# Kernel tuning notes

Measured on AMD Instinct MI355X. Metric: run time of the kernel, lower is better.

The kernel has to match this reference:

```python
import jax, jax.numpy as jnp
import numpy as np

DIM = 512
HEADS = 8


def setup_inputs() -> dict:
    key = jax.random.key(0)
    k1, k2, k3, k4 = jax.random.split(key, 4)
    head_dim = DIM // HEADS
    scale = head_dim ** -0.5
    x = jax.random.normal(k1, (4, 4096, DIM), dtype=jnp.float32)
    Wqkv = jax.random.normal(k2, (3 * DIM, DIM), dtype=jnp.float32) * (DIM ** -0.5)
    temperature = jnp.ones((HEADS, 1, 1), dtype=jnp.float32) * scale
    Wproj = jax.random.normal(k3, (DIM, DIM), dtype=jnp.float32) * (DIM ** -0.5)
    bproj = jnp.zeros((DIM,), dtype=jnp.float32)
    return {"x": x, "Wqkv": Wqkv, "temperature": temperature, "Wproj": Wproj, "bproj": bproj}


def reference(x, Wqkv, temperature, Wproj, bproj):
    B, N, C = x.shape
    H = temperature.shape[0]
    D = C // H
    qkv = (x @ Wqkv.T).reshape(B, N, 3, H, D).transpose(2, 0, 3, 1, 4)  # (3,B,H,N,D)
    q, k, v = qkv[0], qkv[1], qkv[2]
    q = jax.nn.relu(q)
    k = jax.nn.relu(k)
    # denom = clamp(q @ sum_n k, min=100) -> (B,H,N,1)
    ksum = k.sum(axis=2)  # (B,H,D)
    denom = jnp.clip(jnp.einsum('bhnd,bhd->bhn', q, ksum), 100.0)[..., None]
    # attn = (k^T v) * temperature -> (B,H,D,D)
    attn = jnp.einsum('bhnd,bhne->bhde', k, v) * temperature
    attn1 = jnp.einsum('bhnd,bhde->bhne', q, attn)  # (B,H,N,D)
    out = attn1 / denom
    y = out.transpose(0, 2, 1, 3).reshape(B, N, C) @ Wproj.T + bproj
    return (y, attn1)
```

## Files before the change

kernel.cpp:

```cpp
#include <hip/hip_runtime.h>
#include <cstdint>
#include <cstddef>

typedef _Float16 f16;
typedef _Float16 f16x4 __attribute__((ext_vector_type(4)));
typedef _Float16 f16x8 __attribute__((ext_vector_type(8)));
typedef float f32x4 __attribute__((ext_vector_type(4)));

#define MFMA16(a, b, c) __builtin_amdgcn_mfma_f32_16x16x32_f16(a, b, c, 0, 0, 0)

static __device__ __forceinline__ void gld16(const void* g, void* l) {
  __builtin_amdgcn_global_load_lds(
      (const __attribute__((address_space(1))) void*)g,
      (__attribute__((address_space(3))) void*)l, 16, 0, 0);
}

#define B_ 4
#define N_ 4096
#define C_ 512
#define H_ 8
#define D_ 64
#define BN_ROWS 16384
#define QKV_COLS 1536

__global__ __launch_bounds__(256) void k_convert(
    const float* __restrict__ x, const float* __restrict__ wqkv,
    const float* __restrict__ wproj,
    f16* __restrict__ xh, f16* __restrict__ wqkvh, f16* __restrict__ wprojh)
{
  const int NX  = (BN_ROWS * C_) / 4;
  const int NW1 = (QKV_COLS * C_) / 4;
  const int NW2 = (C_ * C_) / 4;
  const int total = NX + NW1 + NW2;
  const int stride = gridDim.x * blockDim.x;
  for (int i = blockIdx.x * blockDim.x + threadIdx.x; i < total; i += stride) {
    const float4* s; f16x4* d; int j;
    if (i < NX)              { s = (const float4*)x;     d = (f16x4*)xh;     j = i; }
    else if (i < NX + NW1)   { s = (const float4*)wqkv;  d = (f16x4*)wqkvh;  j = i - NX; }
    else                     { s = (const float4*)wproj; d = (f16x4*)wprojh; j = i - NX - NW1; }
    float4 v = s[j];
    f16x4 o; o[0] = (f16)v.x; o[1] = (f16)v.y; o[2] = (f16)v.z; o[3] = (f16)v.w;
    d[j] = o;
  }
}

__global__ __launch_bounds__(256) void k_qkv_gemm(
    const f16* __restrict__ X, const f16* __restrict__ W, f16* __restrict__ Out)
{
  __shared__ f16 As[128][64];
  __shared__ f16 Bs[128][64];
  int w = (blockIdx.x & 7) * 192 + (blockIdx.x >> 3);
  const int n0 = (w % 12) * 128;
  const int m0 = (w / 12) * 128;
  const int tid = threadIdx.x;
  const int wid = tid >> 6;
  const int lane = tid & 63;
  const int lr = lane & 15, lg = lane >> 4;
  const int sr = lane >> 3;
  const int sslot = (lane & 7) ^ sr;
  const int wr = (wid >> 1) * 64, wc = (wid & 1) * 64;
  f32x4 acc[4][4] = {};
  for (int kt = 0; kt < 512; kt += 64) {
#pragma unroll
    for (int i = 0; i < 4; ++i) {
      int chunk = wid * 4 + i;
      int row = chunk * 8 + sr;
      gld16(&X[(size_t)(m0 + row) * 512 + kt + sslot * 8], &As[chunk * 8][0]);
      gld16(&W[(size_t)(n0 + row) * 512 + kt + sslot * 8], &Bs[chunk * 8][0]);
    }
    __syncthreads();
#pragma unroll
    for (int kk = 0; kk < 2; ++kk) {
      f16x8 af[4], bf[4];
#pragma unroll
      for (int m = 0; m < 4; ++m)
        af[m] = *(const f16x8*)&As[wr + m * 16 + lr][(((kk * 4 + lg) ^ (lr & 7)) * 8)];
#pragma unroll
      for (int n = 0; n < 4; ++n)
        bf[n] = *(const f16x8*)&Bs[wc + n * 16 + lr][(((kk * 4 + lg) ^ (lr & 7)) * 8)];
#pragma unroll
      for (int m = 0; m < 4; ++m)
#pragma unroll
        for (int n = 0; n < 4; ++n)
          acc[m][n] = MFMA16(bf[n], af[m], acc[m][n]);
    }
    __syncthreads();
  }
#pragma unroll
  for (int m = 0; m < 4; ++m)
#pragma unroll
    for (int n = 0; n < 4; ++n) {
      int row = m0 + wr + m * 16 + lr;
      int col = n0 + wc + n * 16 + lg * 4;
      f16x4 o;
      bool relu = (col < 1024);
#pragma unroll
      for (int j = 0; j < 4; ++j) {
        float v = acc[m][n][j];
        if (relu) v = fmaxf(v, 0.f);
        o[j] = (f16)v;
      }
      *(f16x4*)&Out[(size_t)row * QKV_COLS + col] = o;
    }
}

__global__ __launch_bounds__(256) void k_ktv(
    const f16* __restrict__ qkv, float* __restrict__ partial, float* __restrict__ pksum)
{
  __shared__ f16 ks[32][64];
  __shared__ f16 vs[32][64];
  const int bh = blockIdx.x, sp = blockIdx.y;
  const int b = bh >> 3, h = bh & 7;
  const int tid = threadIdx.x, wid = tid >> 6, lane = tid & 63;
  const int srow = lane >> 3, scol = (lane & 7) * 8;
  const int td = (wid << 2) | (lane >> 4);
  const int te = lane & 15;
  float acc[4][4] = {};
  float ksacc[4] = {0.f, 0.f, 0.f, 0.f};
  const size_t rowbase = (size_t)b * N_ + sp * 128;
  for (int t = 0; t < 4; ++t) {
    int nb = t * 32 + wid * 8 + srow;
    gld16(&qkv[(rowbase + nb) * QKV_COLS + 512 + h * 64 + scol], &ks[wid * 8][0]);
    gld16(&qkv[(rowbase + nb) * QKV_COLS + 1024 + h * 64 + scol], &vs[wid * 8][0]);
    __syncthreads();
#pragma unroll 4
    for (int n = 0; n < 32; ++n) {
      f16x4 kd = *(const f16x4*)&ks[n][td * 4];
      f16x4 ve = *(const f16x4*)&vs[n][te * 4];
      float kf[4], vf[4];
#pragma unroll
      for (int i = 0; i < 4; ++i) { kf[i] = (float)kd[i]; vf[i] = (float)ve[i]; }
#pragma unroll
      for (int i = 0; i < 4; ++i)
#pragma unroll
        for (int j = 0; j < 4; ++j)
          acc[i][j] += kf[i] * vf[j];
      if (te == 0) {
#pragma unroll
        for (int i = 0; i < 4; ++i) ksacc[i] += kf[i];
      }
    }
    __syncthreads();
  }
  float* pp = partial + (size_t)(bh * 32 + sp) * 4096;
#pragma unroll
  for (int i = 0; i < 4; ++i)
#pragma unroll
    for (int j = 0; j < 4; ++j)
      pp[(td * 4 + i) * 64 + te * 4 + j] = acc[i][j];
  if (te == 0) {
    float* kp = pksum + (bh * 32 + sp) * 64;
#pragma unroll
    for (int i = 0; i < 4; ++i) kp[td * 4 + i] = ksacc[i];
  }
}

__global__ __launch_bounds__(256) void k_reduce(
    const float* __restrict__ partial, const float* __restrict__ pksum,
    float* __restrict__ attn_acc, float* __restrict__ ksum)
{
  const int bh = blockIdx.x, seg = blockIdx.y, tid = threadIdx.x;
  const int i = seg * 256 + tid;
  float s = 0.f;
#pragma unroll 8
  for (int sp = 0; sp < 32; ++sp) s += partial[(size_t)(bh * 32 + sp) * 4096 + i];
  attn_acc[bh * 4096 + i] = s;
  if (seg == 0 && tid < 64) {
    float t2 = 0.f;
#pragma unroll 8
    for (int sp = 0; sp < 32; ++sp) t2 += pksum[(bh * 32 + sp) * 64 + tid];
    ksum[bh * 64 + tid] = t2;
  }
}

__global__ __launch_bounds__(256) void k_attn1(
    const f16* __restrict__ qkv, const float* __restrict__ attn_acc,
    const float* __restrict__ ksum, const float* __restrict__ temp,
    float* __restrict__ attn1_out, f16* __restrict__ outh)
{
  __shared__ f16 attnT[64][64];
  __shared__ float ksum_s[64];
  __shared__ float denom_s[256];
  const int bh = blockIdx.x, sp = blockIdx.y;
  const int b = bh >> 3, h = bh & 7;
  const int tid = threadIdx.x, wid = tid >> 6, lane = tid & 63;
  const int lr = lane & 15, lg = lane >> 4;
  const int n0 = sp * 256;
  const float tscale = temp[h];
  {
    int e = tid & 63, dblk = (tid >> 6) * 16;
    float vals[16];
#pragma unroll
    for (int x = 0; x < 16; ++x)
      vals[x] = attn_acc[bh * 4096 + (dblk + x) * 64 + e] * tscale;
#pragma unroll
    for (int half = 0; half < 2; ++half) {
      int slot = ((dblk >> 3) + half) ^ (e & 7);
      f16x8 pk;
#pragma unroll
      for (int j = 0; j < 8; ++j) pk[j] = (f16)vals[half * 8 + j];
      *(f16x8*)&attnT[e][slot * 8] = pk;
    }
  }
  if (tid < 64) ksum_s[tid] = ksum[bh * 64 + tid];
  __syncthreads();
  {
    size_t row = (size_t)b * N_ + n0 + tid;
    const f16* qrow = &qkv[row * QKV_COLS + h * 64];
    float dot = 0.f;
#pragma unroll
    for (int d0 = 0; d0 < 64; d0 += 8) {
      f16x8 qv = *(const f16x8*)&qrow[d0];
#pragma unroll
      for (int j = 0; j < 8; ++j) dot += (float)qv[j] * ksum_s[d0 + j];
    }
    denom_s[tid] = fmaxf(dot, 100.f);
  }
  f16x8 bf[4][2];
#pragma unroll
  for (int et = 0; et < 4; ++et)
#pragma unroll
    for (int kk = 0; kk < 2; ++kk) {
      int e = et * 16 + lr;
      bf[et][kk] = *(const f16x8*)&attnT[e][(((kk * 4 + lg) ^ (e & 7)) * 8)];
    }
  __syncthreads();
  f32x4 acc[4][4] = {};
#pragma unroll
  for (int mt = 0; mt < 4; ++mt) {
    size_t rbase = ((size_t)b * N_ + n0 + wid * 64 + mt * 16 + lr) * QKV_COLS + h * 64;
#pragma unroll
    for (int kk = 0; kk < 2; ++kk) {
      f16x8 a = *(const f16x8*)&qkv[rbase + kk * 32 + lg * 8];
#pragma unroll
      for (int et = 0; et < 4; ++et)
        acc[mt][et] = MFMA16(bf[et][kk], a, acc[mt][et]);
    }
  }
#pragma unroll
  for (int mt = 0; mt < 4; ++mt) {
    int rl = wid * 64 + mt * 16 + lr;
    int n = n0 + rl;
    float dn = denom_s[rl];
#pragma unroll
    for (int et = 0; et < 4; ++et) {
      int e = et * 16 + lg * 4;
      float4 o;
      f16x4 oh;
      o.x = acc[mt][et][0]; o.y = acc[mt][et][1]; o.z = acc[mt][et][2]; o.w = acc[mt][et][3];
#pragma unroll
      for (int j = 0; j < 4; ++j) oh[j] = (f16)(acc[mt][et][j] / dn);
      *(float4*)&attn1_out[((size_t)bh * N_ + n) * 64 + e] = o;
      *(f16x4*)&outh[((size_t)b * N_ + n) * 512 + h * 64 + e] = oh;
    }
  }
}

__global__ __launch_bounds__(256) void k_proj_gemm(
    const f16* __restrict__ X, const f16* __restrict__ W,
    const float* __restrict__ bias, float* __restrict__ Y)
{
  __shared__ f16 As[128][64];
  __shared__ f16 Bs[128][64];
  int w = (blockIdx.x & 7) * 64 + (blockIdx.x >> 3);
  const int n0 = (w % 4) * 128;
  const int m0 = (w / 4) * 128;
  const int tid = threadIdx.x;
  const int wid = tid >> 6;
  const int lane = tid & 63;
  const int lr = lane & 15, lg = lane >> 4;
  const int sr = lane >> 3;
  const int sslot = (lane & 7) ^ sr;
  const int wr = (wid >> 1) * 64, wc = (wid & 1) * 64;
  f32x4 acc[4][4] = {};
  for (int kt = 0; kt < 512; kt += 64) {
#pragma unroll
    for (int i = 0; i < 4; ++i) {
      int chunk = wid * 4 + i;
      int row = chunk * 8 + sr;
      gld16(&X[(size_t)(m0 + row) * 512 + kt + sslot * 8], &As[chunk * 8][0]);
      gld16(&W[(size_t)(n0 + row) * 512 + kt + sslot * 8], &Bs[chunk * 8][0]);
    }
    __syncthreads();
#pragma unroll
    for (int kk = 0; kk < 2; ++kk) {
      f16x8 af[4], bf[4];
#pragma unroll
      for (int m = 0; m < 4; ++m)
        af[m] = *(const f16x8*)&As[wr + m * 16 + lr][(((kk * 4 + lg) ^ (lr & 7)) * 8)];
#pragma unroll
      for (int n = 0; n < 4; ++n)
        bf[n] = *(const f16x8*)&Bs[wc + n * 16 + lr][(((kk * 4 + lg) ^ (lr & 7)) * 8)];
#pragma unroll
      for (int m = 0; m < 4; ++m)
#pragma unroll
        for (int n = 0; n < 4; ++n)
          acc[m][n] = MFMA16(bf[n], af[m], acc[m][n]);
    }
    __syncthreads();
  }
#pragma unroll
  for (int m = 0; m < 4; ++m)
#pragma unroll
    for (int n = 0; n < 4; ++n) {
      int row = m0 + wr + m * 16 + lr;
      int col = n0 + wc + n * 16 + lg * 4;
      float4 o;
      o.x = acc[m][n][0] + bias[col + 0];
      o.y = acc[m][n][1] + bias[col + 1];
      o.z = acc[m][n][2] + bias[col + 2];
      o.w = acc[m][n][3] + bias[col + 3];
      *(float4*)&Y[(size_t)row * C_ + col] = o;
    }
}

extern "C" void kernel_launch(void* const* d_in, const int* in_sizes, int n_in,
                              void* d_out, int out_size, void* d_ws, size_t ws_size,
                              hipStream_t stream)
{
  const float* x     = (const float*)d_in[0];
  const float* wqkv  = (const float*)d_in[1];
  const float* temp  = (const float*)d_in[2];
  const float* wproj = (const float*)d_in[3];
  const float* bproj = (const float*)d_in[4];
  float* y_out     = (float*)d_out;
  float* attn1_out = (float*)d_out + 8388608;

  char* ws = (char*)d_ws;
  f16*   xh       = (f16*)(ws);
  float* partial  = (float*)(ws);
  f16*   wqkvh    = (f16*)(ws + 16777216);
  f16*   wprojh   = (f16*)(ws + 18350080);
  f16*   qkvh     = (f16*)(ws + 18874368);
  float* attn_acc = (float*)(ws + 69206016);
  float* ksum     = (float*)(ws + 69730304);
  float* pksum    = (float*)(ws + 69738496);
  f16*   outh     = (f16*)(ws + 70000640);

  hipLaunchKernelGGL(k_convert,  dim3(2048),    dim3(256), 0, stream, x, wqkv, wproj, xh, wqkvh, wprojh);
  hipLaunchKernelGGL(k_qkv_gemm, dim3(1536),    dim3(256), 0, stream, xh, wqkvh, qkvh);
  hipLaunchKernelGGL(k_ktv,      dim3(32, 32),  dim3(256), 0, stream, qkvh, partial, pksum);
  hipLaunchKernelGGL(k_reduce,   dim3(32, 16),  dim3(256), 0, stream, partial, pksum, attn_acc, ksum);
  hipLaunchKernelGGL(k_attn1,    dim3(32, 16),  dim3(256), 0, stream, qkvh, attn_acc, ksum, temp, attn1_out, outh);
  hipLaunchKernelGGL(k_proj_gemm,dim3(512),     dim3(256), 0, stream, outh, wprojh, bproj, y_out);
}
```

Baseline: 123.1 us.

## Replace both GEMMs with 256x128-tile, 8-wave, 4-slot pipelined templated kernel

Both GEMM kernels are replaced by one templated kernel with 256x128 output tiles, 512 threads and a four-slot LDS ring. Loads are issued two k-steps ahead using direct global-to-LDS transfers, and waiting uses explicit vmcnt counters with a single barrier per step. MFMA sections get raised wave priority. The goal is to hide global load latency and halve the barrier count per k-tile. In exchange the XOR swizzle is dropped, so LDS reads may hit bank conflicts, and the proj GEMM now launches only 256 blocks, which may underfill the GPU.

```diff
diff --git a/kernel.cpp b/kernel.cpp
--- a/kernel.cpp
+++ b/kernel.cpp
@@ -44,64 +44,112 @@
   }
 }
 
-__global__ __launch_bounds__(256) void k_qkv_gemm(
-    const f16* __restrict__ X, const f16* __restrict__ W, f16* __restrict__ Out)
-{
-  __shared__ f16 As[128][64];
-  __shared__ f16 Bs[128][64];
-  int w = (blockIdx.x & 7) * 192 + (blockIdx.x >> 3);
-  const int n0 = (w % 12) * 128;
-  const int m0 = (w / 12) * 128;
+template<int NTN, int BPX, int MODE>
+__global__ __launch_bounds__(512, 2) void k_gemm8(
+    const f16* __restrict__ A, const f16* __restrict__ Bm,
+    const float* __restrict__ bias, f16* __restrict__ OutH,
+    float* __restrict__ OutF)
+{
+  constexpr int BM = 256, BN = 128;
+  constexpr int SLOT = (BM + BN) * 32;
+  __shared__ f16 lds[4 * SLOT];
+
+  int w = (blockIdx.x & 7) * BPX + (blockIdx.x >> 3);
+  const int m0 = (w / NTN) * BM;
+  const int n0 = (w % NTN) * BN;
   const int tid = threadIdx.x;
-  const int wid = tid >> 6;
-  const int lane = tid & 63;
+  const int wid = tid >> 6, lane = tid & 63;
   const int lr = lane & 15, lg = lane >> 4;
-  const int sr = lane >> 3;
-  const int sslot = (lane & 7) ^ sr;
-  const int wr = (wid >> 1) * 64, wc = (wid & 1) * 64;
+  const int wm = wid >> 1, wn = wid & 1;
+
+  const int strow = lane >> 2, stslot = (lane & 3) * 8;
+
   f32x4 acc[4][4] = {};
-  for (int kt = 0; kt < 512; kt += 64) {
-#pragma unroll
-    for (int i = 0; i < 4; ++i) {
-      int chunk = wid * 4 + i;
-      int row = chunk * 8 + sr;
-      gld16(&X[(size_t)(m0 + row) * 512 + kt + sslot * 8], &As[chunk * 8][0]);
-      gld16(&W[(size_t)(n0 + row) * 512 + kt + sslot * 8], &Bs[chunk * 8][0]);
-    }
-    __syncthreads();
-#pragma unroll
-    for (int kk = 0; kk < 2; ++kk) {
-      f16x8 af[4], bf[4];
-#pragma unroll
-      for (int m = 0; m < 4; ++m)
-        af[m] = *(const f16x8*)&As[wr + m * 16 + lr][(((kk * 4 + lg) ^ (lr & 7)) * 8)];
+
+#define STAGE(tt, s)                                                          \
+  do {                                                                        \
+    f16* lbase = lds + (s) * SLOT;                                            \
+    _Pragma("unroll")                                                         \
+    for (int r = 0; r < 2; ++r) {                                             \
+      int row = r * 128 + wid * 16;                                           \
+      gld16(&A[(size_t)(m0 + row + strow) * 512 + (tt) * 32 + stslot],        \
+            lbase + row * 32);                                                \
+    }                                                                         \
+    {                                                                         \
+      int row = wid * 16;                                                     \
+      gld16(&Bm[(size_t)(n0 + row + strow) * 512 + (tt) * 32 + stslot],       \
+            lbase + BM * 32 + row * 32);                                      \
+    }                                                                         \
+  } while (0)
+
+  STAGE(0, 0);
+  STAGE(1, 1);
+  asm volatile("s_waitcnt vmcnt(3)" ::: "memory");
+  __builtin_amdgcn_s_barrier();
+  asm volatile("" ::: "memory");
+
+#pragma unroll
+  for (int t = 0; t < 16; ++t) {
+    if (t + 2 < 16) STAGE(t + 2, (t + 2) & 3);
+    const f16* base = lds + (t & 3) * SLOT;
+    f16x8 af[4], bf[4];
+#pragma unroll
+    for (int m = 0; m < 4; ++m)
+      af[m] = *(const f16x8*)(base + (wm * 64 + m * 16 + lr) * 32 + lg * 8);
+#pragma unroll
+    for (int n = 0; n < 4; ++n)
+      bf[n] = *(const f16x8*)(base + BM * 32 + (wn * 64 + n * 16 + lr) * 32 + lg * 8);
+    __builtin_amdgcn_s_setprio(1);
+#pragma unroll
+    for (int m = 0; m < 4; ++m)
 #pragma unroll
       for (int n = 0; n < 4; ++n)
-        bf[n] = *(const f16x8*)&Bs[wc + n * 16 + lr][(((kk * 4 + lg) ^ (lr & 7)) * 8)];
-#pragma unroll
-      for (int m = 0; m < 4; ++m)
-#pragma unroll
-        for (int n = 0; n < 4; ++n)
-          acc[m][n] = MFMA16(bf[n], af[m], acc[m][n]);
-    }
-    __syncthreads();
-  }
-#pragma unroll
-  for (int m = 0; m < 4; ++m)
-#pragma unroll
-    for (int n = 0; n < 4; ++n) {
-      int row = m0 + wr + m * 16 + lr;
-      int col = n0 + wc + n * 16 + lg * 4;
-      f16x4 o;
-      bool relu = (col < 1024);
-#pragma unroll
-      for (int j = 0; j < 4; ++j) {
-        float v = acc[m][n][j];
-        if (relu) v = fmaxf(v, 0.f);
-        o[j] = (f16)v;
+        acc[m][n] = MFMA16(bf[n], af[m], acc[m][n]);
+    __builtin_amdgcn_s_setprio(0);
+    if (t < 14) {
+      asm volatile("s_waitcnt vmcnt(3)" ::: "memory");
+    } else if (t == 14) {
+      asm volatile("s_waitcnt vmcnt(0)" ::: "memory");
+    }
+    if (t < 15) {
+      __builtin_amdgcn_s_barrier();
+      asm volatile("" ::: "memory");
+    }
+  }
+#undef STAGE
+
+  if (MODE == 0) {
+    const bool relu = (n0 < 1024);
+#pragma unroll
+    for (int m = 0; m < 4; ++m)
+#pragma unroll
+      for (int n = 0; n < 4; ++n) {
+        int row = m0 + wm * 64 + m * 16 + lr;
+        int col = n0 + wn * 64 + n * 16 + lg * 4;
+        f16x4 o;
+#pragma unroll
+        for (int j = 0; j < 4; ++j) {
+          float v = acc[m][n][j];
+          if (relu) v = fmaxf(v, 0.f);
+          o[j] = (f16)v;
+        }
+        *(f16x4*)&OutH[(size_t)row * QKV_COLS + col] = o;
       }
-      *(f16x4*)&Out[(size_t)row * QKV_COLS + col] = o;
-    }
+  } else {
+#pragma unroll
+    for (int m = 0; m < 4; ++m)
+#pragma unroll
+      for (int n = 0; n < 4; ++n) {
+        int row = m0 + wm * 64 + m * 16 + lr;
+        int col = n0 + wn * 64 + n * 16 + lg * 4;
+        float4 o;
+        o.x = acc[m][n][0] + bias[col + 0];
+        o.y = acc[m][n][1] + bias[col + 1];
+        o.z = acc[m][n][2] + bias[col + 2];
+        o.w = acc[m][n][3] + bias[col + 3];
+        *(float4*)&OutF[(size_t)row * C_ + col] = o;
+      }
+  }
 }
 
 __global__ __launch_bounds__(256) void k_ktv(
@@ -256,64 +304,6 @@
   }
 }
 
-__global__ __launch_bounds__(256) void k_proj_gemm(
-    const f16* __restrict__ X, const f16* __restrict__ W,
-    const float* __restrict__ bias, float* __restrict__ Y)
-{
-  __shared__ f16 As[128][64];
-  __shared__ f16 Bs[128][64];
-  int w = (blockIdx.x & 7) * 64 + (blockIdx.x >> 3);
-  const int n0 = (w % 4) * 128;
-  const int m0 = (w / 4) * 128;
-  const int tid = threadIdx.x;
-  const int wid = tid >> 6;
-  const int lane = tid & 63;
-  const int lr = lane & 15, lg = lane >> 4;
-  const int sr = lane >> 3;
-  const int sslot = (lane & 7) ^ sr;
-  const int wr = (wid >> 1) * 64, wc = (wid & 1) * 64;
-  f32x4 acc[4][4] = {};
-  for (int kt = 0; kt < 512; kt += 64) {
-#pragma unroll
-    for (int i = 0; i < 4; ++i) {
-      int chunk = wid * 4 + i;
-      int row = chunk * 8 + sr;
-      gld16(&X[(size_t)(m0 + row) * 512 + kt + sslot * 8], &As[chunk * 8][0]);
-      gld16(&W[(size_t)(n0 + row) * 512 + kt + sslot * 8], &Bs[chunk * 8][0]);
-    }
-    __syncthreads();
-#pragma unroll
-    for (int kk = 0; kk < 2; ++kk) {
-      f16x8 af[4], bf[4];
-#pragma unroll
-      for (int m = 0; m < 4; ++m)
-        af[m] = *(const f16x8*)&As[wr + m * 16 + lr][(((kk * 4 + lg) ^ (lr & 7)) * 8)];
-#pragma unroll
-      for (int n = 0; n < 4; ++n)
-        bf[n] = *(const f16x8*)&Bs[wc + n * 16 + lr][(((kk * 4 + lg) ^ (lr & 7)) * 8)];
-#pragma unroll
-      for (int m = 0; m < 4; ++m)
-#pragma unroll
-        for (int n = 0; n < 4; ++n)
-          acc[m][n] = MFMA16(bf[n], af[m], acc[m][n]);
-    }
-    __syncthreads();
-  }
-#pragma unroll
-  for (int m = 0; m < 4; ++m)
-#pragma unroll
-    for (int n = 0; n < 4; ++n) {
-      int row = m0 + wr + m * 16 + lr;
-      int col = n0 + wc + n * 16 + lg * 4;
-      float4 o;
-      o.x = acc[m][n][0] + bias[col + 0];
-      o.y = acc[m][n][1] + bias[col + 1];
-      o.z = acc[m][n][2] + bias[col + 2];
-      o.w = acc[m][n][3] + bias[col + 3];
-      *(float4*)&Y[(size_t)row * C_ + col] = o;
-    }
-}
-
 extern "C" void kernel_launch(void* const* d_in, const int* in_sizes, int n_in,
                               void* d_out, int out_size, void* d_ws, size_t ws_size,
                               hipStream_t stream)
@@ -338,9 +328,11 @@
   f16*   outh     = (f16*)(ws + 70000640);
 
   hipLaunchKernelGGL(k_convert,  dim3(2048),    dim3(256), 0, stream, x, wqkv, wproj, xh, wqkvh, wprojh);
-  hipLaunchKernelGGL(k_qkv_gemm, dim3(1536),    dim3(256), 0, stream, xh, wqkvh, qkvh);
+  hipLaunchKernelGGL((k_gemm8<12, 96, 0>), dim3(768), dim3(512), 0, stream,
+                     xh, wqkvh, (const float*)nullptr, qkvh, (float*)nullptr);
   hipLaunchKernelGGL(k_ktv,      dim3(32, 32),  dim3(256), 0, stream, qkvh, partial, pksum);
   hipLaunchKernelGGL(k_reduce,   dim3(32, 16),  dim3(256), 0, stream, partial, pksum, attn_acc, ksum);
   hipLaunchKernelGGL(k_attn1,    dim3(32, 16),  dim3(256), 0, stream, qkvh, attn_acc, ksum, temp, attn1_out, outh);
-  hipLaunchKernelGGL(k_proj_gemm,dim3(512),     dim3(256), 0, stream, outh, wprojh, bproj, y_out);
-}
+  hipLaunchKernelGGL((k_gemm8<4, 32, 1>), dim3(256), dim3(512), 0, stream,
+                     outh, wprojh, bproj, (f16*)nullptr, y_out);
+}
```

Measured after the change: 128.4 us. 1.04x slower.

## Fuse fp32-to-fp16 x conversion into QKV GEMM and double-buffer both GEMMs

Applied to the files above, without the earlier changes.

The QKV GEMM now reads fp32 x directly into registers, converts it to fp16 and writes it to swizzled LDS. This removes the separate conversion pass over x, which wrote a 16 MB fp16 copy and then read it back. Both GEMMs gain double-buffered LDS with prefetch of the next K tile while MFMAs run on the current one. They also use manual waitcnt/barrier control and setprio around the MFMA block. The trade-off is more LDS per block (64 KB), register-staged A loads in the QKV GEMM, and fragile hand-written vmcnt accounting.

```diff
diff --git a/kernel.cpp b/kernel.cpp
--- a/kernel.cpp
+++ b/kernel.cpp
@@ -24,76 +24,127 @@
 #define QKV_COLS 1536
 
 __global__ __launch_bounds__(256) void k_convert(
-    const float* __restrict__ x, const float* __restrict__ wqkv,
-    const float* __restrict__ wproj,
-    f16* __restrict__ xh, f16* __restrict__ wqkvh, f16* __restrict__ wprojh)
-{
-  const int NX  = (BN_ROWS * C_) / 4;
+    const float* __restrict__ wqkv, const float* __restrict__ wproj,
+    f16* __restrict__ wqkvh, f16* __restrict__ wprojh)
+{
   const int NW1 = (QKV_COLS * C_) / 4;
   const int NW2 = (C_ * C_) / 4;
-  const int total = NX + NW1 + NW2;
+  const int total = NW1 + NW2;
   const int stride = gridDim.x * blockDim.x;
   for (int i = blockIdx.x * blockDim.x + threadIdx.x; i < total; i += stride) {
     const float4* s; f16x4* d; int j;
-    if (i < NX)              { s = (const float4*)x;     d = (f16x4*)xh;     j = i; }
-    else if (i < NX + NW1)   { s = (const float4*)wqkv;  d = (f16x4*)wqkvh;  j = i - NX; }
-    else                     { s = (const float4*)wproj; d = (f16x4*)wprojh; j = i - NX - NW1; }
+    if (i < NW1) { s = (const float4*)wqkv;  d = (f16x4*)wqkvh;  j = i; }
+    else         { s = (const float4*)wproj; d = (f16x4*)wprojh; j = i - NW1; }
     float4 v = s[j];
     f16x4 o; o[0] = (f16)v.x; o[1] = (f16)v.y; o[2] = (f16)v.z; o[3] = (f16)v.w;
     d[j] = o;
   }
 }
 
-__global__ __launch_bounds__(256) void k_qkv_gemm(
-    const f16* __restrict__ X, const f16* __restrict__ W, f16* __restrict__ Out)
-{
-  __shared__ f16 As[128][64];
-  __shared__ f16 Bs[128][64];
+__global__ __launch_bounds__(256, 2) void k_qkv_gemm(
+    const float* __restrict__ X, const f16* __restrict__ W, f16* __restrict__ Out)
+{
+  __shared__ f16 As[2][128][64];
+  __shared__ f16 Bs[2][128][64];
   int w = (blockIdx.x & 7) * 192 + (blockIdx.x >> 3);
+  const int m0 = (w / 12) * 128;
   const int n0 = (w % 12) * 128;
-  const int m0 = (w / 12) * 128;
   const int tid = threadIdx.x;
-  const int wid = tid >> 6;
-  const int lane = tid & 63;
+  const int wid = tid >> 6, lane = tid & 63;
   const int lr = lane & 15, lg = lane >> 4;
-  const int sr = lane >> 3;
-  const int sslot = (lane & 7) ^ sr;
-  const int wr = (wid >> 1) * 64, wc = (wid & 1) * 64;
+  const int wm = wid >> 1, wn = wid & 1;
+  const int sr = lane >> 3, sslot = (lane & 7) ^ sr;
+  const int arow = tid >> 1;
+  const float* asrc = &X[(size_t)(m0 + arow) * 512 + (tid & 1) * 32];
+  float4 areg[8];
   f32x4 acc[4][4] = {};
-  for (int kt = 0; kt < 512; kt += 64) {
-#pragma unroll
-    for (int i = 0; i < 4; ++i) {
-      int chunk = wid * 4 + i;
-      int row = chunk * 8 + sr;
-      gld16(&X[(size_t)(m0 + row) * 512 + kt + sslot * 8], &As[chunk * 8][0]);
-      gld16(&W[(size_t)(n0 + row) * 512 + kt + sslot * 8], &Bs[chunk * 8][0]);
-    }
-    __syncthreads();
+
+#define STAGE_B(tt, q)                                                        \
+  do {                                                                        \
+    _Pragma("unroll")                                                         \
+    for (int i = 0; i < 4; ++i) {                                             \
+      int chunk = wid * 4 + i;                                                \
+      gld16(&W[(size_t)(n0 + chunk * 8 + sr) * 512 + (tt) * 64 + sslot * 8],  \
+            &Bs[q][chunk * 8][0]);                                            \
+    }                                                                         \
+  } while (0)
+#define LOADA(tt)                                                             \
+  do {                                                                        \
+    _Pragma("unroll")                                                         \
+    for (int j = 0; j < 8; ++j)                                               \
+      areg[j] = *(const float4*)(asrc + (tt) * 64 + j * 4);                   \
+  } while (0)
+#define WRITEA(q)                                                             \
+  do {                                                                        \
+    _Pragma("unroll")                                                         \
+    for (int p2 = 0; p2 < 4; ++p2) {                                          \
+      int slot = (tid & 1) * 4 + p2;                                          \
+      f16x8 pk;                                                               \
+      pk[0] = (f16)areg[2*p2].x;   pk[1] = (f16)areg[2*p2].y;                 \
+      pk[2] = (f16)areg[2*p2].z;   pk[3] = (f16)areg[2*p2].w;                 \
+      pk[4] = (f16)areg[2*p2+1].x; pk[5] = (f16)areg[2*p2+1].y;               \
+      pk[6] = (f16)areg[2*p2+1].z; pk[7] = (f16)areg[2*p2+1].w;               \
+      *(f16x8*)&As[q][arow][((slot ^ (arow & 7)) * 8)] = pk;                  \
+    }                                                                         \
+  } while (0)
+
+  STAGE_B(0, 0);
+  LOADA(0);
+  asm volatile("s_waitcnt vmcnt(0)" ::: "memory");
+  WRITEA(0);
+  LOADA(1);
+  asm volatile("s_waitcnt lgkmcnt(0)" ::: "memory");
+  __builtin_amdgcn_s_barrier();
+  asm volatile("" ::: "memory");
+
+#pragma unroll
+  for (int t = 0; t < 8; ++t) {
+    const int p = t & 1, q = p ^ 1;
+    if (t < 7) STAGE_B(t + 1, q);
+    f16x8 af[2][4], bf[2][4];
 #pragma unroll
     for (int kk = 0; kk < 2; ++kk) {
-      f16x8 af[4], bf[4];
 #pragma unroll
       for (int m = 0; m < 4; ++m)
-        af[m] = *(const f16x8*)&As[wr + m * 16 + lr][(((kk * 4 + lg) ^ (lr & 7)) * 8)];
+        af[kk][m] = *(const f16x8*)&As[p][wm * 64 + m * 16 + lr][(((kk * 4 + lg) ^ (lr & 7)) * 8)];
 #pragma unroll
       for (int n = 0; n < 4; ++n)
-        bf[n] = *(const f16x8*)&Bs[wc + n * 16 + lr][(((kk * 4 + lg) ^ (lr & 7)) * 8)];
+        bf[kk][n] = *(const f16x8*)&Bs[p][wn * 64 + n * 16 + lr][(((kk * 4 + lg) ^ (lr & 7)) * 8)];
+    }
+    if (t < 7) {
+      asm volatile("s_waitcnt vmcnt(4)" ::: "memory");
+      WRITEA(q);
+      if (t < 6) LOADA(t + 2);
+    }
+    __builtin_amdgcn_s_setprio(1);
+#pragma unroll
+    for (int kk = 0; kk < 2; ++kk)
 #pragma unroll
       for (int m = 0; m < 4; ++m)
 #pragma unroll
         for (int n = 0; n < 4; ++n)
-          acc[m][n] = MFMA16(bf[n], af[m], acc[m][n]);
-    }
-    __syncthreads();
-  }
+          acc[m][n] = MFMA16(bf[kk][n], af[kk][m], acc[m][n]);
+    __builtin_amdgcn_s_setprio(0);
+    if (t < 7) {
+      asm volatile("s_waitcnt lgkmcnt(0)" ::: "memory");
+      if (t < 6) asm volatile("s_waitcnt vmcnt(8)" ::: "memory");
+      else       asm volatile("s_waitcnt vmcnt(0)" ::: "memory");
+      __builtin_amdgcn_s_barrier();
+      asm volatile("" ::: "memory");
+    }
+  }
+#undef STAGE_B
+#undef LOADA
+#undef WRITEA
+
+  const bool relu = (n0 < 1024);
 #pragma unroll
   for (int m = 0; m < 4; ++m)
 #pragma unroll
     for (int n = 0; n < 4; ++n) {
-      int row = m0 + wr + m * 16 + lr;
-      int col = n0 + wc + n * 16 + lg * 4;
+      int row = m0 + wm * 64 + m * 16 + lr;
+      int col = n0 + wn * 64 + n * 16 + lg * 4;
       f16x4 o;
-      bool relu = (col < 1024);
 #pragma unroll
       for (int j = 0; j < 4; ++j) {
         float v = acc[m][n][j];
@@ -256,55 +307,77 @@
   }
 }
 
-__global__ __launch_bounds__(256) void k_proj_gemm(
-    const f16* __restrict__ X, const f16* __restrict__ W,
+__global__ __launch_bounds__(256, 2) void k_proj_gemm(
+    const f16* __restrict__ Xh, const f16* __restrict__ W,
     const float* __restrict__ bias, float* __restrict__ Y)
 {
-  __shared__ f16 As[128][64];
-  __shared__ f16 Bs[128][64];
+  __shared__ f16 As[2][128][64];
+  __shared__ f16 Bs[2][128][64];
   int w = (blockIdx.x & 7) * 64 + (blockIdx.x >> 3);
+  const int m0 = (w / 4) * 128;
   const int n0 = (w % 4) * 128;
-  const int m0 = (w / 4) * 128;
   const int tid = threadIdx.x;
-  const int wid = tid >> 6;
-  const int lane = tid & 63;
+  const int wid = tid >> 6, lane = tid & 63;
   const int lr = lane & 15, lg = lane >> 4;
-  const int sr = lane >> 3;
-  const int sslot = (lane & 7) ^ sr;
-  const int wr = (wid >> 1) * 64, wc = (wid & 1) * 64;
+  const int wm = wid >> 1, wn = wid & 1;
+  const int sr = lane >> 3, sslot = (lane & 7) ^ sr;
   f32x4 acc[4][4] = {};
-  for (int kt = 0; kt < 512; kt += 64) {
-#pragma unroll
-    for (int i = 0; i < 4; ++i) {
-      int chunk = wid * 4 + i;
-      int row = chunk * 8 + sr;
-      gld16(&X[(size_t)(m0 + row) * 512 + kt + sslot * 8], &As[chunk * 8][0]);
-      gld16(&W[(size_t)(n0 + row) * 512 + kt + sslot * 8], &Bs[chunk * 8][0]);
-    }
-    __syncthreads();
+
+#define STAGE8(tt, q)                                                         \
+  do {                                                                        \
+    _Pragma("unroll")                                                         \
+    for (int i = 0; i < 4; ++i) {                                             \
+      int chunk = wid * 4 + i;                                                \
+      gld16(&Xh[(size_t)(m0 + chunk * 8 + sr) * 512 + (tt) * 64 + sslot * 8], \
+            &As[q][chunk * 8][0]);                                            \
+      gld16(&W[(size_t)(n0 + chunk * 8 + sr) * 512 + (tt) * 64 + sslot * 8],  \
+            &Bs[q][chunk * 8][0]);                                            \
+    }                                                                         \
+  } while (0)
+
+  STAGE8(0, 0);
+  asm volatile("s_waitcnt vmcnt(0)" ::: "memory");
+  __builtin_amdgcn_s_barrier();
+  asm volatile("" ::: "memory");
+
+#pragma unroll
+  for (int t = 0; t < 8; ++t) {
+    const int p = t & 1, q = p ^ 1;
+    if (t < 7) STAGE8(t + 1, q);
+    f16x8 af[2][4], bf[2][4];
 #pragma unroll
     for (int kk = 0; kk < 2; ++kk) {
-      f16x8 af[4], bf[4];
 #pragma unroll
       for (int m = 0; m < 4; ++m)
-        af[m] = *(const f16x8*)&As[wr + m * 16 + lr][(((kk * 4 + lg) ^ (lr & 7)) * 8)];
+        af[kk][m] = *(const f16x8*)&As[p][wm * 64 + m * 16 + lr][(((kk * 4 + lg) ^ (lr & 7)) * 8)];
 #pragma unroll
       for (int n = 0; n < 4; ++n)
-        bf[n] = *(const f16x8*)&Bs[wc + n * 16 + lr][(((kk * 4 + lg) ^ (lr & 7)) * 8)];
+        bf[kk][n] = *(const f16x8*)&Bs[p][wn * 64 + n * 16 + lr][(((kk * 4 + lg) ^ (lr & 7)) * 8)];
+    }
+    __builtin_amdgcn_s_setprio(1);
+#pragma unroll
+    for (int kk = 0; kk < 2; ++kk)
 #pragma unroll
       for (int m = 0; m < 4; ++m)
 #pragma unroll
         for (int n = 0; n < 4; ++n)
-          acc[m][n] = MFMA16(bf[n], af[m], acc[m][n]);
-    }
-    __syncthreads();
-  }
+          acc[m][n] = MFMA16(bf[kk][n], af[kk][m], acc[m][n]);
+    __builtin_amdgcn_s_setprio(0);
+    if (t < 7) {
+      asm volatile("s_waitcnt lgkmcnt(0)" ::: "memory");
+      asm volatile("s_waitcnt vmcnt(0)" ::: "memory");
+      __builtin_amdgcn_s_barrier();
+      asm volatile("" ::: "memory");
+    }
+  }
+#undef STAGE8
+
 #pragma unroll
   for (int m = 0; m < 4; ++m)
 #pragma unroll
     for (int n = 0; n < 4; ++n) {
-      int row = m0 + wr + m * 16 + lr;
-      int col = n0 + wc + n * 16 + lg * 4;
+      int row = m0 + wm * 64 + m * 16 + lr;
+      int col = n0 + wn * 64 + n * 16 + lg * 4;
       float4 o;
       o.x = acc[m][n][0] + bias[col + 0];
       o.y = acc[m][n][1] + bias[col + 1];
@@ -327,7 +400,6 @@
   float* attn1_out = (float*)d_out + 8388608;
 
   char* ws = (char*)d_ws;
-  f16*   xh       = (f16*)(ws);
   float* partial  = (float*)(ws);
   f16*   wqkvh    = (f16*)(ws + 16777216);
   f16*   wprojh   = (f16*)(ws + 18350080);
@@ -337,8 +409,8 @@
   float* pksum    = (float*)(ws + 69738496);
   f16*   outh     = (f16*)(ws + 70000640);
 
-  hipLaunchKernelGGL(k_convert,  dim3(2048),    dim3(256), 0, stream, x, wqkv, wproj, xh, wqkvh, wprojh);
-  hipLaunchKernelGGL(k_qkv_gemm, dim3(1536),    dim3(256), 0, stream, xh, wqkvh, qkvh);
+  hipLaunchKernelGGL(k_convert,  dim3(512),     dim3(256), 0, stream, wqkv, wproj, wqkvh, wprojh);
+  hipLaunchKernelGGL(k_qkv_gemm, dim3(1536),    dim3(256), 0, stream, x, wqkvh, qkvh);
   hipLaunchKernelGGL(k_ktv,      dim3(32, 32),  dim3(256), 0, stream, qkvh, partial, pksum);
   hipLaunchKernelGGL(k_reduce,   dim3(32, 16),  dim3(256), 0, stream, partial, pksum, attn_acc, ksum);
   hipLaunchKernelGGL(k_attn1,    dim3(32, 16),  dim3(256), 0, stream, qkvh, attn_acc, ksum, temp, attn1_out, outh);
```

New measurement: 146.5 us. 19.0% more time.

## Fuse attention-output and projection GEMM into one kernel keeping output in LDS

Applied to the files above, without the earlier changes.

Merges k_attn1 and k_proj_gemm into a single kernel. Each block handles 64 rows of one batch across all 8 heads, and the normalized per-head output is kept in a 64x512 f16 LDS tile. The projection then runs directly from that tile while Wproj chunks are double-buffered in LDS, which removes the f16 outh round trip through global memory and one launch. The cost is only 256 blocks with a large LDS footprint (launch bounds min 1 block per SIMD group), so each CU holds one block and occupancy is low. Every block also re-reads the full Wproj.

```diff
diff --git a/kernel.cpp b/kernel.cpp
--- a/kernel.cpp
+++ b/kernel.cpp
@@ -173,144 +173,184 @@
   }
 }
 
-__global__ __launch_bounds__(256) void k_attn1(
+__global__ __launch_bounds__(256, 1) void k_attn_proj(
     const f16* __restrict__ qkv, const float* __restrict__ attn_acc,
     const float* __restrict__ ksum, const float* __restrict__ temp,
-    float* __restrict__ attn1_out, f16* __restrict__ outh)
+    const f16* __restrict__ Wp, const float* __restrict__ bias,
+    float* __restrict__ attn1_out, float* __restrict__ Y)
 {
   __shared__ f16 attnT[64][64];
-  __shared__ float ksum_s[64];
-  __shared__ float denom_s[256];
-  const int bh = blockIdx.x, sp = blockIdx.y;
-  const int b = bh >> 3, h = bh & 7;
-  const int tid = threadIdx.x, wid = tid >> 6, lane = tid & 63;
+  __shared__ f16 qs[64][64];
+  __shared__ f16 outs[64][512];
+  __shared__ f16 Bs[2][256][64];
+  __shared__ float ksum_s[512];
+  __shared__ float bias_s[512];
+  __shared__ float denom_s[64];
+
+  const int bid = blockIdx.x;
+  const int b = bid >> 6, sp = bid & 63;
+  const size_t gr = (size_t)b * N_ + sp * 64;
+  const int tid = threadIdx.x;
+  const int wid = tid >> 6, lane = tid & 63;
   const int lr = lane & 15, lg = lane >> 4;
-  const int n0 = sp * 256;
-  const float tscale = temp[h];
-  {
-    int e = tid & 63, dblk = (tid >> 6) * 16;
-    float vals[16];
-#pragma unroll
-    for (int x = 0; x < 16; ++x)
-      vals[x] = attn_acc[bh * 4096 + (dblk + x) * 64 + e] * tscale;
-#pragma unroll
-    for (int half = 0; half < 2; ++half) {
-      int slot = ((dblk >> 3) + half) ^ (e & 7);
-      f16x8 pk;
-#pragma unroll
-      for (int j = 0; j < 8; ++j) pk[j] = (f16)vals[half * 8 + j];
-      *(f16x8*)&attnT[e][slot * 8] = pk;
-    }
-  }
-  if (tid < 64) ksum_s[tid] = ksum[bh * 64 + tid];
+  const int sr = lane >> 3, sslot = (lane & 7) ^ sr;
+
+  ksum_s[tid]       = ksum[b * 512 + tid];
+  ksum_s[tid + 256] = ksum[b * 512 + tid + 256];
+  bias_s[tid]       = bias[tid];
+  bias_s[tid + 256] = bias[tid + 256];
+
+  for (int h = 0; h < 8; ++h) {
+    const float tsc = temp[h];
+    {
+      int e = tid & 63, dblk = (tid >> 6) * 16;
+      float vals[16];
+#pragma unroll
+      for (int x = 0; x < 16; ++x)
+        vals[x] = attn_acc[(size_t)(b * 8 + h) * 4096 + (dblk + x) * 64 + e] * tsc;
+#pragma unroll
+      for (int half = 0; half < 2; ++half) {
+        int slot = ((dblk >> 3) + half) ^ (e & 7);
+        f16x8 pk;
+#pragma unroll
+        for (int j = 0; j < 8; ++j) pk[j] = (f16)vals[half * 8 + j];
+        *(f16x8*)&attnT[e][slot * 8] = pk;
+      }
+    }
+#pragma unroll
+    for (int rr = 0; rr < 2; ++rr) {
+      int row = rr * 32 + wid * 8;
+      gld16(&qkv[(gr + row + sr) * QKV_COLS + h * 64 + sslot * 8], &qs[row][0]);
+    }
+    __syncthreads();
+    if (tid < 64) {
+      int r = tid;
+      float dot = 0.f;
+#pragma unroll
+      for (int c = 0; c < 8; ++c) {
+        f16x8 qv = *(const f16x8*)&qs[r][((c ^ (r & 7)) * 8)];
+#pragma unroll
+        for (int j = 0; j < 8; ++j) dot += (float)qv[j] * ksum_s[h * 64 + c * 8 + j];
+      }
+      denom_s[r] = fmaxf(dot, 100.f);
+    }
+    const int arow = wid * 16 + lr;
+    f16x8 af[2], bf[4][2];
+#pragma unroll
+    for (int kk = 0; kk < 2; ++kk)
+      af[kk] = *(const f16x8*)&qs[arow][(((kk * 4 + lg) ^ (lr & 7)) * 8)];
+#pragma unroll
+    for (int et = 0; et < 4; ++et)
+#pragma unroll
+      for (int kk = 0; kk < 2; ++kk)
+        bf[et][kk] = *(const f16x8*)&attnT[et * 16 + lr][(((kk * 4 + lg) ^ (lr & 7)) * 8)];
+    f32x4 acc1[4] = {};
+#pragma unroll
+    for (int kk = 0; kk < 2; ++kk)
+#pragma unroll
+      for (int et = 0; et < 4; ++et)
+        acc1[et] = MFMA16(bf[et][kk], af[kk], acc1[et]);
+    __syncthreads();
+    {
+      const int rl = wid * 16 + lr;
+      const float dn = denom_s[rl];
+#pragma unroll
+      for (int et = 0; et < 4; ++et) {
+        int e = et * 16 + lg * 4;
+        float4 o;
+        o.x = acc1[et][0]; o.y = acc1[et][1]; o.z = acc1[et][2]; o.w = acc1[et][3];
+        *(float4*)&attn1_out[((size_t)(b * 8 + h) * N_ + sp * 64 + rl) * 64 + e] = o;
+        f16x4 oh;
+#pragma unroll
+        for (int j = 0; j < 4; ++j) oh[j] = (f16)(acc1[et][j] / dn);
+        int c = h * 64 + e;
+        *(f16x4*)((char*)&outs[0][0] + rl * 1024 +
+                  (((c >> 3) ^ (rl & 7)) * 16) + (lg & 1) * 8) = oh;
+      }
+    }
+  }
   __syncthreads();
-  {
-    size_t row = (size_t)b * N_ + n0 + tid;
-    const f16* qrow = &qkv[row * QKV_COLS + h * 64];
-    float dot = 0.f;
-#pragma unroll
-    for (int d0 = 0; d0 < 64; d0 += 8) {
-      f16x8 qv = *(const f16x8*)&qrow[d0];
-#pragma unroll
-      for (int j = 0; j < 8; ++j) dot += (float)qv[j] * ksum_s[d0 + j];
-    }
-    denom_s[tid] = fmaxf(dot, 100.f);
-  }
-  f16x8 bf[4][2];
-#pragma unroll
-  for (int et = 0; et < 4; ++et)
-#pragma unroll
-    for (int kk = 0; kk < 2; ++kk) {
-      int e = et * 16 + lr;
-      bf[et][kk] = *(const f16x8*)&attnT[e][(((kk * 4 + lg) ^ (e & 7)) * 8)];
-    }
+
+  f32x4 accP0[4][4] = {};
+  f32x4 accP1[4][4] = {};
+
+#define STAGEP(hf_, kc_, bufi)                                                \
+  do {                                                                        \
+    _Pragma("unroll")                                                         \
+    for (int rd = 0; rd < 8; ++rd) {                                          \
+      int row = rd * 32 + wid * 8;                                            \
+      gld16(&Wp[(size_t)((hf_) * 256 + row + sr) * 512 + (kc_) * 64 + sslot * 8], \
+            &Bs[bufi][row][0]);                                               \
+    }                                                                         \
+  } while (0)
+
+  STAGEP(0, 0, 0);
   __syncthreads();
-  f32x4 acc[4][4] = {};
-#pragma unroll
-  for (int mt = 0; mt < 4; ++mt) {
-    size_t rbase = ((size_t)b * N_ + n0 + wid * 64 + mt * 16 + lr) * QKV_COLS + h * 64;
-#pragma unroll
-    for (int kk = 0; kk < 2; ++kk) {
-      f16x8 a = *(const f16x8*)&qkv[rbase + kk * 32 + lg * 8];
-#pragma unroll
-      for (int et = 0; et < 4; ++et)
-        acc[mt][et] = MFMA16(bf[et][kk], a, acc[mt][et]);
-    }
-  }
-#pragma unroll
-  for (int mt = 0; mt < 4; ++mt) {
-    int rl = wid * 64 + mt * 16 + lr;
-    int n = n0 + rl;
-    float dn = denom_s[rl];
-#pragma unroll
-    for (int et = 0; et < 4; ++et) {
-      int e = et * 16 + lg * 4;
-      float4 o;
-      f16x4 oh;
-      o.x = acc[mt][et][0]; o.y = acc[mt][et][1]; o.z = acc[mt][et][2]; o.w = acc[mt][et][3];
-#pragma unroll
-      for (int j = 0; j < 4; ++j) oh[j] = (f16)(acc[mt][et][j] / dn);
-      *(float4*)&attn1_out[((size_t)bh * N_ + n) * 64 + e] = o;
-      *(f16x4*)&outh[((size_t)b * N_ + n) * 512 + h * 64 + e] = oh;
-    }
-  }
-}
-
-__global__ __launch_bounds__(256) void k_proj_gemm(
-    const f16* __restrict__ X, const f16* __restrict__ W,
-    const float* __restrict__ bias, float* __restrict__ Y)
-{
-  __shared__ f16 As[128][64];
-  __shared__ f16 Bs[128][64];
-  int w = (blockIdx.x & 7) * 64 + (blockIdx.x >> 3);
-  const int n0 = (w % 4) * 128;
-  const int m0 = (w / 4) * 128;
-  const int tid = threadIdx.x;
-  const int wid = tid >> 6;
-  const int lane = tid & 63;
-  const int lr = lane & 15, lg = lane >> 4;
-  const int sr = lane >> 3;
-  const int sslot = (lane & 7) ^ sr;
-  const int wr = (wid >> 1) * 64, wc = (wid & 1) * 64;
-  f32x4 acc[4][4] = {};
-  for (int kt = 0; kt < 512; kt += 64) {
-#pragma unroll
-    for (int i = 0; i < 4; ++i) {
-      int chunk = wid * 4 + i;
-      int row = chunk * 8 + sr;
-      gld16(&X[(size_t)(m0 + row) * 512 + kt + sslot * 8], &As[chunk * 8][0]);
-      gld16(&W[(size_t)(n0 + row) * 512 + kt + sslot * 8], &Bs[chunk * 8][0]);
-    }
-    __syncthreads();
-#pragma unroll
-    for (int kk = 0; kk < 2; ++kk) {
-      f16x8 af[4], bf[4];
-#pragma unroll
-      for (int m = 0; m < 4; ++m)
-        af[m] = *(const f16x8*)&As[wr + m * 16 + lr][(((kk * 4 + lg) ^ (lr & 7)) * 8)];
-#pragma unroll
-      for (int n = 0; n < 4; ++n)
-        bf[n] = *(const f16x8*)&Bs[wc + n * 16 + lr][(((kk * 4 + lg) ^ (lr & 7)) * 8)];
-#pragma unroll
-      for (int m = 0; m < 4; ++m)
+
+  for (int kc = 0; kc < 8; ++kc) {
+    STAGEP(1, kc, 1);
+    f16x8 afp[2][4];
+#pragma unroll
+    for (int kk = 0; kk < 2; ++kk)
+#pragma unroll
+      for (int m = 0; m < 4; ++m) {
+        int row = m * 16 + lr;
+        afp[kk][m] = *(const f16x8*)((const char*)&outs[0][0] + row * 1024 +
+                      (((kc * 8 + kk * 4 + lg) ^ (row & 7)) * 16));
+      }
+    {
+      f16x8 bfp[4];
+#pragma unroll
+      for (int kk = 0; kk < 2; ++kk) {
 #pragma unroll
         for (int n = 0; n < 4; ++n)
-          acc[m][n] = MFMA16(bf[n], af[m], acc[m][n]);
-    }
-    __syncthreads();
-  }
+          bfp[n] = *(const f16x8*)&Bs[0][wid * 64 + n * 16 + lr][(((kk * 4 + lg) ^ (lr & 7)) * 8)];
+#pragma unroll
+        for (int m = 0; m < 4; ++m)
+#pragma unroll
+          for (int n = 0; n < 4; ++n)
+            accP0[m][n] = MFMA16(bfp[n], afp[kk][m], accP0[m][n]);
+      }
+    }
+    __syncthreads();
+    if (kc < 7) STAGEP(0, kc + 1, 0);
+    {
+      f16x8 bfp[4];
+#pragma unroll
+      for (int kk = 0; kk < 2; ++kk) {
+#pragma unroll
+        for (int n = 0; n < 4; ++n)
+          bfp[n] = *(const f16x8*)&Bs[1][wid * 64 + n * 16 + lr][(((kk * 4 + lg) ^ (lr & 7)) * 8)];
+#pragma unroll
+        for (int m = 0; m < 4; ++m)
+#pragma unroll
+          for (int n = 0; n < 4; ++n)
+            accP1[m][n] = MFMA16(bfp[n], afp[kk][m], accP1[m][n]);
+      }
+    }
+    __syncthreads();
+  }
+#undef STAGEP
+
 #pragma unroll
   for (int m = 0; m < 4; ++m)
 #pragma unroll
     for (int n = 0; n < 4; ++n) {
-      int row = m0 + wr + m * 16 + lr;
-      int col = n0 + wc + n * 16 + lg * 4;
-      float4 o;
-      o.x = acc[m][n][0] + bias[col + 0];
-      o.y = acc[m][n][1] + bias[col + 1];
-      o.z = acc[m][n][2] + bias[col + 2];
-      o.w = acc[m][n][3] + bias[col + 3];
-      *(float4*)&Y[(size_t)row * C_ + col] = o;
+      size_t row = gr + m * 16 + lr;
+      int col0 = wid * 64 + n * 16 + lg * 4;
+      float4 o0;
+      o0.x = accP0[m][n][0] + bias_s[col0 + 0];
+      o0.y = accP0[m][n][1] + bias_s[col0 + 1];
+      o0.z = accP0[m][n][2] + bias_s[col0 + 2];
+      o0.w = accP0[m][n][3] + bias_s[col0 + 3];
+      *(float4*)&Y[row * C_ + col0] = o0;
+      int col1 = col0 + 256;
+      float4 o1;
+      o1.x = accP1[m][n][0] + bias_s[col1 + 0];
+      o1.y = accP1[m][n][1] + bias_s[col1 + 1];
+      o1.z = accP1[m][n][2] + bias_s[col1 + 2];
+      o1.w = accP1[m][n][3] + bias_s[col1 + 3];
+      *(float4*)&Y[row * C_ + col1] = o1;
     }
 }
 
@@ -335,12 +375,11 @@
   float* attn_acc = (float*)(ws + 69206016);
   float* ksum     = (float*)(ws + 69730304);
   float* pksum    = (float*)(ws + 69738496);
-  f16*   outh     = (f16*)(ws + 70000640);
-
-  hipLaunchKernelGGL(k_convert,  dim3(2048),    dim3(256), 0, stream, x, wqkv, wproj, xh, wqkvh, wprojh);
-  hipLaunchKernelGGL(k_qkv_gemm, dim3(1536),    dim3(256), 0, stream, xh, wqkvh, qkvh);
-  hipLaunchKernelGGL(k_ktv,      dim3(32, 32),  dim3(256), 0, stream, qkvh, partial, pksum);
-  hipLaunchKernelGGL(k_reduce,   dim3(32, 16),  dim3(256), 0, stream, partial, pksum, attn_acc, ksum);
-  hipLaunchKernelGGL(k_attn1,    dim3(32, 16),  dim3(256), 0, stream, qkvh, attn_acc, ksum, temp, attn1_out, outh);
-  hipLaunchKernelGGL(k_proj_gemm,dim3(512),     dim3(256), 0, stream, outh, wprojh, bproj, y_out);
-}
+
+  hipLaunchKernelGGL(k_convert,   dim3(2048),   dim3(256), 0, stream, x, wqkv, wproj, xh, wqkvh, wprojh);
+  hipLaunchKernelGGL(k_qkv_gemm,  dim3(1536),   dim3(256), 0, stream, xh, wqkvh, qkvh);
+  hipLaunchKernelGGL(k_ktv,       dim3(32, 32), dim3(256), 0, stream, qkvh, partial, pksum);
+  hipLaunchKernelGGL(k_reduce,    dim3(32, 16), dim3(256), 0, stream, partial, pksum, attn_acc, ksum);
+  hipLaunchKernelGGL(k_attn_proj, dim3(256),    dim3(256), 0, stream,
+                     qkvh, attn_acc, ksum, temp, wprojh, bproj, attn1_out, y_out);
+}
```

Result: no change. 121.2 us (-1.5%).
